# Kernel optimization log

Hardware: AMD Instinct MI355X
Metric: run time of the kernel (lower is better)

Reference implementation:

```python
import jax, jax.numpy as jnp
import numpy as np

B = 4096
D = 512
N_I = 1000000
N_T = 1000000
GAMMA = 0.8
EPS = 1e-10
RHO_I = 8.0
RHO_T = 8.0
ETA_INIT = 1e-05
BETA_U = 0.5
GRAD_CLIP = 5.0
TAU_MIN, TAU_MAX = 0.005, 0.05
TAU_INIT = 0.01


def setup_inputs() -> dict:
    key = jax.random.key(0)
    k1, k2 = jax.random.split(key)
    img = jax.random.normal(k1, (B, D), jnp.float32)
    txt = jax.random.normal(k2, (B, D), jnp.float32)
    # CLIP-style L2-normalized features
    img = img / jnp.linalg.norm(img, axis=1, keepdims=True)
    txt = txt / jnp.linalg.norm(txt, axis=1, keepdims=True)
    return {
        "image_features": img,
        "text_features": txt,
        "s_I": jnp.zeros(N_I, jnp.float32),
        "s_T": jnp.zeros(N_T, jnp.float32),
        "b_I": jnp.zeros(N_I, jnp.float32),
        "b_T": jnp.zeros(N_T, jnp.float32),
        "u_I": jnp.zeros(N_I, jnp.float32),
        "u_T": jnp.zeros(N_T, jnp.float32),
        "tau_I": jnp.full((N_I,), TAU_INIT, jnp.float32),
        "tau_T": jnp.full((N_T,), TAU_INIT, jnp.float32),
        "image_ids": jnp.arange(B, dtype=jnp.int32),
        "text_ids": jnp.arange(B, dtype=jnp.int32),
        "epoch": 1,
    }


def reference(image_features, text_features, s_I, s_T, b_I, b_T, u_I, u_T,
              tau_I, tau_T, image_ids, text_ids, epoch):
    sg = jax.lax.stop_gradient
    sim = jnp.einsum('id,jd->ij', image_features, text_features)  # [B,B]
    diag = jnp.diagonal(sim)
    Bn = sim.shape[0]
    tau_img = tau_I[image_ids]  # [B]
    tau_txt = tau_T[text_ids]   # [B]
    image_diffs = sim - diag[:, None]
    text_diffs = sim - diag[None, :]
    # .detach() in the original -> stop_gradient here
    idt = sg(image_diffs / tau_img[:, None])
    tdt = sg(text_diffs / tau_txt[None, :])
    old_b_I = b_I[image_ids]
    old_b_T = b_T[text_ids]
    # running max for log-sum-exp stabilization
    b_I_row = jnp.maximum(idt.max(axis=1), old_b_I)
    b_T_col = jnp.maximum(tdt.max(axis=0), old_b_T)
    b_I_new = b_I.at[image_ids].set(b_I_row)
    b_T_new = b_T.at[text_ids].set(b_T_col)
    mask = 1.0 - jnp.eye(Bn, dtype=sim.dtype)
    exp_i = jnp.exp(idt - b_I_row[:, None]) * mask
    exp_t = jnp.exp(tdt - b_T_col[None, :]) * mask
    g_I = exp_i.sum(axis=1)
    g_T = exp_t.sum(axis=0)
    if epoch == 0:
        sI = g_I
        sT = g_T
    else:
        sI = (1.0 - GAMMA) * s_I[image_ids] * jnp.exp(old_b_I - b_I_row) + GAMMA * g_I
        sT = (1.0 - GAMMA) * s_T[text_ids] * jnp.exp(old_b_T - b_T_col) + GAMMA * g_T
    s_I_new = s_I.at[image_ids].set(sI)
    s_T_new = s_T.at[text_ids].set(sT)
    w_i = sg(exp_i / (sI[:, None] + EPS))
    w_t = sg(exp_t / (sT[None, :] + EPS))
    image_loss = (w_i * image_diffs).sum(axis=1)
    text_loss = (w_t * text_diffs).sum(axis=0)
    total_loss = image_loss.mean() + text_loss.mean()
    tw_i = jnp.log(sI / (Bn - 1)) + b_I_row + RHO_I - (w_i * idt).sum(axis=1)
    tw_t = jnp.log(sT / (Bn - 1)) + b_T_col + RHO_T - (w_t * tdt).sum(axis=0)
    # torch uses in-place clamp_ on a view, so the returned means are clipped
    tw_i = jnp.clip(tw_i, -GRAD_CLIP, GRAD_CLIP)
    tw_t = jnp.clip(tw_t, -GRAD_CLIP, GRAD_CLIP)
    u_I_val = (1.0 - BETA_U) * u_I[image_ids] + BETA_U * tw_i
    u_T_val = (1.0 - BETA_U) * u_T[text_ids] + BETA_U * tw_t
    u_I_new = u_I.at[image_ids].set(u_I_val)
    u_T_new = u_T.at[text_ids].set(u_T_val)
    tau_I_new = tau_I.at[image_ids].set(jnp.clip(tau_img - ETA_INIT * u_I_val, TAU_MIN, TAU_MAX))
    tau_T_new = tau_T.at[text_ids].set(jnp.clip(tau_txt - ETA_INIT * u_T_val, TAU_MIN, TAU_MAX))
    return (total_loss, tau_img.mean(), tau_txt.mean(), tw_i.mean(), tw_t.mean(),
            s_I_new, s_T_new, b_I_new, b_T_new, u_I_new, u_T_new, tau_I_new, tau_T_new)
```

## Files before the change

kernel.cpp:

```cpp
#include <hip/hip_runtime.h>

typedef unsigned short u16;
typedef unsigned int u32;

typedef __bf16 bf16x8 __attribute__((ext_vector_type(8)));
typedef float floatx4 __attribute__((ext_vector_type(4)));

__device__ __forceinline__ u16 f2bf(float f) {
    union { float f; u32 u; } c; c.f = f;
    u32 u = c.u;
    u32 r = u + 0x7FFFu + ((u >> 16) & 1u);
    return (u16)(r >> 16);
}
__device__ __forceinline__ float bf2f(u16 x) {
    union { u32 u; float f; } c; c.u = ((u32)x) << 16; return c.f;
}

__device__ __forceinline__ void comb(float& M, float& P0, float& P1,
                                     float m, float p0, float p1) {
    float nm = fmaxf(M, m);
    float s = __expf(M - nm), t = __expf(m - nm);
    P0 = P0 * s + p0 * t;
    P1 = P1 * s + p1 * t;
    M = nm;
}

__global__ __launch_bounds__(256) void presplit(
    const float* __restrict__ a, const float* __restrict__ b,
    u16* __restrict__ Ah, u16* __restrict__ Al,
    u16* __restrict__ Bh, u16* __restrict__ Bl, int n,
    const float* __restrict__ tauI, const float* __restrict__ tauT,
    const int* __restrict__ img_ids, const int* __restrict__ txt_ids,
    float* __restrict__ taur, float* __restrict__ tauc) {
    if (blockIdx.y == 0 && blockIdx.x < 16) {
        int t = blockIdx.x * 256 + threadIdx.x;
        taur[t] = tauI[img_ids[t]];
        tauc[t] = tauT[txt_ids[t]];
    }
    const float* src = blockIdx.y ? b : a;
    u16* dh = blockIdx.y ? Bh : Ah;
    u16* dl = blockIdx.y ? Bl : Al;
    int i = (blockIdx.x * 256 + threadIdx.x) * 8;
    if (i >= n) return;
    float4 v0 = *(const float4*)&src[i];
    float4 v1 = *(const float4*)&src[i + 4];
    float xs[8] = {v0.x, v0.y, v0.z, v0.w, v1.x, v1.y, v1.z, v1.w};
    u16 h[8], l[8];
#pragma unroll
    for (int e = 0; e < 8; e++) {
        h[e] = f2bf(xs[e]);
        l[e] = f2bf(xs[e] - bf2f(h[e]));
    }
    int r = i >> 9, k = i & 511;
    int off = (((r >> 4) << 4) + (k >> 5)) * 512 + ((((k >> 3) & 3) << 4) + (r & 15)) * 8;
    *(uint4*)&dh[off] = *(uint4*)h;
    *(uint4*)&dl[off] = *(uint4*)l;
}

#define COPY_BLOCKS 2048

__global__ __launch_bounds__(256) void gemm_flash(
    const u16* __restrict__ Ah, const u16* __restrict__ Al,
    const u16* __restrict__ Bh, const u16* __restrict__ Bl,
    const float* __restrict__ taur, const float* __restrict__ tauc,
    float* __restrict__ rowpart, float* __restrict__ colpart,
    float* __restrict__ diag,
    const float* __restrict__ p0, const float* __restrict__ p1,
    const float* __restrict__ p2, const float* __restrict__ p3,
    const float* __restrict__ p4, const float* __restrict__ p5,
    const float* __restrict__ p6, const float* __restrict__ p7,
    float* __restrict__ out, long long n) {
    __shared__ float redbuf[1536];

    const int bid = blockIdx.x;
    if (bid >= 1024) {
        const int cb = bid - 1024;
        const int k = cb >> 8, blk = cb & 255;
        const float* srcs[8] = {p0, p1, p2, p3, p4, p5, p6, p7};
        const float* src = srcs[k];
        float* dst = out + 5 + (size_t)k * (size_t)n;
        const long long G = (n - 3) >> 2;
        for (long long g = (long long)blk * 256 + threadIdx.x; g < G;
             g += 256 * 256) {
            long long e = 3 + 4 * g;
            float4 q = {src[e], src[e + 1], src[e + 2], src[e + 3]};
            *(float4*)&dst[e] = q;
        }
        if (blk == 0) {
            int t = threadIdx.x;
            long long tail0 = 3 + 4 * G;
            int tcount = (int)(n - tail0);
            if (t < 3) dst[t] = src[t];
            else if (t < 3 + tcount) dst[tail0 + (t - 3)] = src[tail0 + (t - 3)];
        }
        return;
    }

    const int tid  = threadIdx.x;
    const int wave = tid >> 6, lane = tid & 63;
    const int lr = lane & 15, quad = lane >> 4;
    const int waveM = wave >> 1, waveN = wave & 1;
    const int x = bid & 7, s = bid >> 3;
    const int rowtile = (x >> 2) * 16 + (s >> 3);
    const int coltile = (x & 3) * 8 + (s & 7);
    const int rowBase = rowtile * 128;
    const int colBase = coltile * 128;

    const size_t baseA = ((size_t)((rowBase >> 4) + waveM * 4)) * 8192 + lane * 8;
    const size_t baseB = ((size_t)((colBase >> 4) + waveN * 4)) * 8192 + lane * 8;

    floatx4 acc[4][4];
#pragma unroll
    for (int mi = 0; mi < 4; mi++)
#pragma unroll
        for (int ni = 0; ni < 4; ni++) acc[mi][ni] = (floatx4)0.0f;

#pragma unroll 2
    for (int tk = 0; tk < 16; tk++) {
        bf16x8 afh[4], afl[4], bfh[4], bfl[4];
#pragma unroll
        for (int mi = 0; mi < 4; mi++) {
            size_t off = baseA + (size_t)mi * 8192 + tk * 512;
            afh[mi] = *(const bf16x8*)&Ah[off];
            afl[mi] = *(const bf16x8*)&Al[off];
        }
#pragma unroll
        for (int ni = 0; ni < 4; ni++) {
            size_t off = baseB + (size_t)ni * 8192 + tk * 512;
            bfh[ni] = *(const bf16x8*)&Bh[off];
            bfl[ni] = *(const bf16x8*)&Bl[off];
        }
#pragma unroll
        for (int mi = 0; mi < 4; mi++)
#pragma unroll
            for (int ni = 0; ni < 4; ni++) {
                acc[mi][ni] = __builtin_amdgcn_mfma_f32_16x16x32_bf16(afh[mi], bfh[ni], acc[mi][ni], 0, 0, 0);
                acc[mi][ni] = __builtin_amdgcn_mfma_f32_16x16x32_bf16(afh[mi], bfl[ni], acc[mi][ni], 0, 0, 0);
                acc[mi][ni] = __builtin_amdgcn_mfma_f32_16x16x32_bf16(afl[mi], bfh[ni], acc[mi][ni], 0, 0, 0);
            }
    }


    if (rowtile == coltile && waveM == waveN) {
#pragma unroll
        for (int mi = 0; mi < 4; mi++)
#pragma unroll
            for (int r = 0; r < 4; r++)
                if (lr == quad * 4 + r)
                    diag[colBase + waveN * 64 + mi * 16 + lr] = acc[mi][mi][r];
    }

#pragma unroll
    for (int mi = 0; mi < 4; mi++) {
#pragma unroll
        for (int r = 0; r < 4; r++) {
            int row_local = waveM * 64 + mi * 16 + quad * 4 + r;
            float vmax = fmaxf(fmaxf(acc[mi][0][r], acc[mi][1][r]),
                               fmaxf(acc[mi][2][r], acc[mi][3][r]));
#pragma unroll
            for (int mask = 1; mask <= 8; mask <<= 1)
                vmax = fmaxf(vmax, __shfl_xor(vmax, mask));
            float it = 1.0f / taur[rowBase + row_local];
            float M = vmax * it;
            float P0 = 0.f, P1 = 0.f;
#pragma unroll
            for (int ni = 0; ni < 4; ni++) {
                float y = acc[mi][ni][r] * it;
                float e = __expf(y - M);
                P0 += e;
                P1 += y * e;
            }
#pragma unroll
            for (int mask = 1; mask <= 8; mask <<= 1) {
                P0 += __shfl_xor(P0, mask);
                P1 += __shfl_xor(P1, mask);
            }
            if (lr == 0) {
                int xx = (row_local * 2 + waveN) * 3;
                redbuf[xx] = M; redbuf[xx + 1] = P0; redbuf[xx + 2] = P1;
            }
        }
    }

#pragma unroll
    for (int ni = 0; ni < 4; ni++) {
        int col_local = waveN * 64 + ni * 16 + lr;
        float vmax = -3.4e38f;
#pragma unroll
        for (int mi = 0; mi < 4; mi++)
            vmax = fmaxf(vmax,
                fmaxf(fmaxf(acc[mi][ni][0], acc[mi][ni][1]),
                      fmaxf(acc[mi][ni][2], acc[mi][ni][3])));
#pragma unroll
        for (int mask = 16; mask <= 32; mask <<= 1)
            vmax = fmaxf(vmax, __shfl_xor(vmax, mask));
        float it = 1.0f / tauc[colBase + col_local];
        float M = vmax * it;
        float P0 = 0.f, P1 = 0.f;
#pragma unroll
        for (int mi = 0; mi < 4; mi++)
#pragma unroll
            for (int r = 0; r < 4; r++) {
                float y = acc[mi][ni][r] * it;
                float e = __expf(y - M);
                P0 += e;
                P1 += y * e;
            }
#pragma unroll
        for (int mask = 16; mask <= 32; mask <<= 1) {
            P0 += __shfl_xor(P0, mask);
            P1 += __shfl_xor(P1, mask);
        }
        if (quad == 0) {
            int xx = 768 + (col_local * 2 + waveM) * 3;
            redbuf[xx] = M; redbuf[xx + 1] = P0; redbuf[xx + 2] = P1;
        }
    }
    __syncthreads();

    if (tid < 128) {
        int xx = tid * 6;
        float M = redbuf[xx], P0 = redbuf[xx + 1], P1 = redbuf[xx + 2];
        comb(M, P0, P1, redbuf[xx + 3], redbuf[xx + 4], redbuf[xx + 5]);
        float* dst = &rowpart[(size_t)(rowBase + tid) * 96 + coltile * 3];
        dst[0] = M; dst[1] = P0; dst[2] = P1;
    } else {
        int c = tid - 128;
        int xx = 768 + c * 6;
        float M = redbuf[xx], P0 = redbuf[xx + 1], P1 = redbuf[xx + 2];
        comb(M, P0, P1, redbuf[xx + 3], redbuf[xx + 4], redbuf[xx + 5]);
        float* dst = &colpart[(size_t)(colBase + c) * 96 + rowtile * 3];
        dst[0] = M; dst[1] = P0; dst[2] = P1;
    }
}

struct FinArgs {
    const float* rowpart; const float* colpart; const float* diag;
    const float* tauI; const float* sI; const float* bI; const float* uI;
    const float* tauT; const float* sT; const float* bT; const float* uT;
    const int* img_ids; const int* txt_ids; const int* epoch_p;
    float* out; float* rowbuf; long long n;
};

__global__ __launch_bounds__(256) void rows_final(FinArgs a) {
    int t = blockIdx.x * 256 + threadIdx.x;
    int side = t >> 12, i = t & 4095;
    const float* part   = side ? a.colpart : a.rowpart;
    const int*   ids    = side ? a.txt_ids : a.img_ids;
    const float* tau_in = side ? a.tauT : a.tauI;
    const float* s_in   = side ? a.sT   : a.sI;
    const float* b_in   = side ? a.bT   : a.bI;
    const float* u_in   = side ? a.uT   : a.uI;

    const float* p = part + (size_t)i * 96;
    float M = -3.4e38f, P0 = 0.f, P1 = 0.f;
#pragma unroll 4
    for (int k = 0; k < 32; k++)
        comb(M, P0, P1, p[3 * k], p[3 * k + 1], p[3 * k + 2]);

    const int id = ids[i];
    const float tau   = tau_in[id];
    const float old_b = b_in[id];
    const float old_s = s_in[id];
    const float old_u = u_in[id];
    const float y_ii  = a.diag[i] / tau;

    float b_row = fmaxf(M - y_ii, old_b);
    float e  = expf(M - y_ii - b_row);
    float S0 = P0 * e - expf(-b_row);
    float S1 = (P1 - y_ii * P0) * e;

    float g = S0;
    float sI = (*a.epoch_p == 0) ? g
             : 0.2f * old_s * expf(old_b - b_row) + 0.8f * g;
    float denom = sI + 1e-10f;
    float wsum = S1 / denom;
    float lossr = tau * wsum;
    float tw = logf(sI * (1.0f / 4095.0f)) + b_row + 8.0f - wsum;
    tw = fminf(fmaxf(tw, -5.0f), 5.0f);
    float uval = 0.5f * old_u + 0.5f * tw;
    float taun = fminf(fmaxf(tau - 1e-5f * uval, 0.005f), 0.05f);

    float* sect = a.out + 5;
    sect[(size_t)(0 + side) * (size_t)a.n + id] = sI;
    sect[(size_t)(2 + side) * (size_t)a.n + id] = b_row;
    sect[(size_t)(4 + side) * (size_t)a.n + id] = uval;
    sect[(size_t)(6 + side) * (size_t)a.n + id] = taun;

    a.rowbuf[(2 * side + 0) * 4096 + i] = lossr;
    a.rowbuf[(2 * side + 1) * 4096 + i] = tw;
}

__global__ __launch_bounds__(256) void scalars(
    const float* __restrict__ rows,
    const float* __restrict__ tau_I, const float* __restrict__ tau_T,
    const int* __restrict__ image_ids, const int* __restrict__ text_ids,
    float* __restrict__ out) {
    int tid = threadIdx.x;
    int lane = tid & 63, wv = tid >> 6;
    float a[6] = {0, 0, 0, 0, 0, 0};
    for (int e = tid; e < 4096; e += 256) {
        a[0] += rows[0 * 4096 + e];
        a[1] += rows[1 * 4096 + e];
        a[2] += rows[2 * 4096 + e];
        a[3] += rows[3 * 4096 + e];
        a[4] += tau_I[image_ids[e]];
        a[5] += tau_T[text_ids[e]];
    }
    __shared__ float sred[4][6];
#pragma unroll
    for (int k = 0; k < 6; k++)
        for (int o = 32; o > 0; o >>= 1) a[k] += __shfl_xor(a[k], o);
    if (lane == 0)
#pragma unroll
        for (int k = 0; k < 6; k++) sred[wv][k] = a[k];
    __syncthreads();
    if (tid == 0) {
#pragma unroll
        for (int k = 0; k < 6; k++)
            a[k] = sred[0][k] + sred[1][k] + sred[2][k] + sred[3][k];
        const float inv = 1.0f / 4096.0f;
        out[0] = (a[0] + a[2]) * inv;
        out[1] = a[4] * inv;
        out[2] = a[5] * inv;
        out[3] = a[1] * inv;
        out[4] = a[3] * inv;
    }
}

extern "C" void kernel_launch(void* const* d_in, const int* in_sizes, int n_in,
                              void* d_out, int out_size, void* d_ws, size_t ws_size,
                              hipStream_t stream) {
    const float* img   = (const float*)d_in[0];
    const float* txt   = (const float*)d_in[1];
    const float* s_I   = (const float*)d_in[2];
    const float* s_T   = (const float*)d_in[3];
    const float* b_I   = (const float*)d_in[4];
    const float* b_T   = (const float*)d_in[5];
    const float* u_I   = (const float*)d_in[6];
    const float* u_T   = (const float*)d_in[7];
    const float* tau_I = (const float*)d_in[8];
    const float* tau_T = (const float*)d_in[9];
    const int* image_ids = (const int*)d_in[10];
    const int* text_ids  = (const int*)d_in[11];
    const int* epoch     = (const int*)d_in[12];
    float* out = (float*)d_out;
    const long long n = in_sizes[2];
    const int nfeat = in_sizes[0];

    const size_t MB = 1024 * 1024;
    u16* Ah = (u16*)d_ws;
    u16* Al = Ah + (size_t)nfeat;
    u16* Bh = Al + (size_t)nfeat;
    u16* Bl = Bh + (size_t)nfeat;
    float* rowpart = (float*)((char*)d_ws + 16 * MB);
    float* colpart = (float*)((char*)d_ws + 18 * MB);
    float* diag    = (float*)((char*)d_ws + 20 * MB);
    float* taur    = (float*)((char*)d_ws + 20 * MB + 256 * 1024);
    float* tauc    = (float*)((char*)d_ws + 20 * MB + 512 * 1024);
    float* rows    = (float*)((char*)d_ws + 21 * MB);

    presplit<<<dim3((nfeat / 8 + 255) / 256, 2), 256, 0, stream>>>(
        img, txt, Ah, Al, Bh, Bl, nfeat,
        tau_I, tau_T, image_ids, text_ids, taur, tauc);

    gemm_flash<<<1024 + COPY_BLOCKS, 256, 0, stream>>>(
        Ah, Al, Bh, Bl, taur, tauc, rowpart, colpart, diag,
        s_I, s_T, b_I, b_T, u_I, u_T, tau_I, tau_T, out, n);

    FinArgs fa;
    fa.rowpart = rowpart; fa.colpart = colpart; fa.diag = diag;
    fa.tauI = tau_I; fa.sI = s_I; fa.bI = b_I; fa.uI = u_I;
    fa.tauT = tau_T; fa.sT = s_T; fa.bT = b_T; fa.uT = u_T;
    fa.img_ids = image_ids; fa.txt_ids = text_ids; fa.epoch_p = epoch;
    fa.out = out; fa.rowbuf = rows; fa.n = n;
    rows_final<<<32, 256, 0, stream>>>(fa);

    scalars<<<1, 256, 0, stream>>>(rows, tau_I, tau_T, image_ids, text_ids, out);
}
```

Measured before the change: 202.1 us.

## Stage GEMM tiles through LDS and interleave state copy with MFMA loop

Operand tiles for the split-bf16 GEMM are now double-buffered in shared memory using global_load_lds, replacing per-wave direct global loads that each wave fetched redundantly. The separate 2048 copy-only blocks are removed, and the bulk copy of the eight million-entry state arrays is spread across the GEMM blocks' K-loop iterations so its memory traffic overlaps the MFMA work. Launch bounds request two blocks per CU, and the final row reduction loads partials as float4 into registers before combining. The 64KB+ shared footprint and added copy work per block may limit occupancy, and the copy now depends on GEMM progress.

```diff
diff --git a/kernel.cpp b/kernel.cpp
--- a/kernel.cpp
+++ b/kernel.cpp
@@ -23,6 +23,12 @@
     P0 = P0 * s + p0 * t;
     P1 = P1 * s + p1 * t;
     M = nm;
+}
+
+__device__ __forceinline__ void gload16(const void* g, void* l) {
+    __builtin_amdgcn_global_load_lds(
+        (const __attribute__((address_space(1))) void*)g,
+        (__attribute__((address_space(3))) void*)l, 16, 0, 0);
 }
 
 __global__ __launch_bounds__(256) void presplit(
@@ -57,9 +63,7 @@
     *(uint4*)&dl[off] = *(uint4*)l;
 }
 
-#define COPY_BLOCKS 2048
-
-__global__ __launch_bounds__(256) void gemm_flash(
+__global__ __launch_bounds__(256, 2) void gemm_flash(
     const u16* __restrict__ Ah, const u16* __restrict__ Al,
     const u16* __restrict__ Bh, const u16* __restrict__ Bl,
     const float* __restrict__ taur, const float* __restrict__ tauc,
@@ -70,32 +74,10 @@
     const float* __restrict__ p4, const float* __restrict__ p5,
     const float* __restrict__ p6, const float* __restrict__ p7,
     float* __restrict__ out, long long n) {
+    __shared__ u16 tiles[32768];
     __shared__ float redbuf[1536];
 
-    const int bid = blockIdx.x;
-    if (bid >= 1024) {
-        const int cb = bid - 1024;
-        const int k = cb >> 8, blk = cb & 255;
-        const float* srcs[8] = {p0, p1, p2, p3, p4, p5, p6, p7};
-        const float* src = srcs[k];
-        float* dst = out + 5 + (size_t)k * (size_t)n;
-        const long long G = (n - 3) >> 2;
-        for (long long g = (long long)blk * 256 + threadIdx.x; g < G;
-             g += 256 * 256) {
-            long long e = 3 + 4 * g;
-            float4 q = {src[e], src[e + 1], src[e + 2], src[e + 3]};
-            *(float4*)&dst[e] = q;
-        }
-        if (blk == 0) {
-            int t = threadIdx.x;
-            long long tail0 = 3 + 4 * G;
-            int tcount = (int)(n - tail0);
-            if (t < 3) dst[t] = src[t];
-            else if (t < 3 + tcount) dst[tail0 + (t - 3)] = src[tail0 + (t - 3)];
-        }
-        return;
-    }
-
+    const int bid  = blockIdx.x;
     const int tid  = threadIdx.x;
     const int wave = tid >> 6, lane = tid & 63;
     const int lr = lane & 15, quad = lane >> 4;
@@ -106,8 +88,17 @@
     const int rowBase = rowtile * 128;
     const int colBase = coltile * 128;
 
-    const size_t baseA = ((size_t)((rowBase >> 4) + waveM * 4)) * 8192 + lane * 8;
-    const size_t baseB = ((size_t)((colBase >> 4) + waveN * 4)) * 8192 + lane * 8;
+    const u16* gb = (wave == 0) ? Ah : (wave == 1) ? Al : (wave == 2) ? Bh : Bl;
+    const int sbase = (wave < 2) ? rowBase : colBase;
+
+#define STAGE(slice, bufb)                                                    \
+    {                                                                         \
+        _Pragma("unroll")                                                     \
+        for (int j = 0; j < 8; j++) {                                         \
+            size_t ge = ((size_t)(sbase + j * 16 + (slice))) * 512 + lane * 8;\
+            gload16(gb + ge, &tiles[(bufb) + (wave * 8 + j) * 512]);          \
+        }                                                                     \
+    }
 
     floatx4 acc[4][4];
 #pragma unroll
@@ -115,30 +106,75 @@
 #pragma unroll
         for (int ni = 0; ni < 4; ni++) acc[mi][ni] = (floatx4)0.0f;
 
-#pragma unroll 2
-    for (int tk = 0; tk < 16; tk++) {
-        bf16x8 afh[4], afl[4], bfh[4], bfl[4];
-#pragma unroll
-        for (int mi = 0; mi < 4; mi++) {
-            size_t off = baseA + (size_t)mi * 8192 + tk * 512;
-            afh[mi] = *(const bf16x8*)&Ah[off];
-            afl[mi] = *(const bf16x8*)&Al[off];
-        }
-#pragma unroll
-        for (int ni = 0; ni < 4; ni++) {
-            size_t off = baseB + (size_t)ni * 8192 + tk * 512;
-            bfh[ni] = *(const bf16x8*)&Bh[off];
-            bfl[ni] = *(const bf16x8*)&Bl[off];
-        }
-#pragma unroll
-        for (int mi = 0; mi < 4; mi++)
+    const int Gq = (int)((n - 3) >> 2);
+    float* dst5 = out + 5;
+
+    STAGE(0, 0)
+
+    if (bid == 0 && tid < 32) {
+        int arr = tid >> 2, j = tid & 3;
+        const float* sp = (arr & 4) ? ((arr & 2) ? ((arr & 1) ? p7 : p6) : ((arr & 1) ? p5 : p4))
+                                    : ((arr & 2) ? ((arr & 1) ? p3 : p2) : ((arr & 1) ? p1 : p0));
+        float* dp = dst5 + (size_t)arr * (size_t)n;
+        long long tail0 = 3 + 4 * (long long)Gq;
+        if (j < 3) dp[j] = sp[j];
+        else
+            for (long long z = tail0; z < n; z++) dp[z] = sp[z];
+    }
+    __syncthreads();
+
+#pragma unroll 1
+    for (int t = 0; t < 16; t++) {
+        const int cb = (t & 1) << 14;
+        const int nb = cb ^ 16384;
+        if (t < 15) STAGE(t + 1, nb)
+
+        bool docopy = false;
+        float c0 = 0.f, c1 = 0.f, c2 = 0.f, c3 = 0.f;
+        int ck = 0; long long ce = 0;
+        if (t < 8) {
+            int c = bid * 256 + tid + t * 262144;
+            ck = c >> 18;
+            int g = c & 262143;
+            if (g < Gq) {
+                docopy = true;
+                ce = 3 + 4 * (long long)g;
+                const float* sp = (ck & 4) ? ((ck & 2) ? ((ck & 1) ? p7 : p6) : ((ck & 1) ? p5 : p4))
+                                           : ((ck & 2) ? ((ck & 1) ? p3 : p2) : ((ck & 1) ? p1 : p0));
+                c0 = sp[ce]; c1 = sp[ce + 1]; c2 = sp[ce + 2]; c3 = sp[ce + 3];
+            }
+        }
+
+        {
+            const int ab = cb + lane * 8;
+            bf16x8 afh[4], afl[4], bfh[4], bfl[4];
+#pragma unroll
+            for (int mi = 0; mi < 4; mi++) {
+                afh[mi] = *(const bf16x8*)&tiles[ab + (waveM * 4 + mi) * 512];
+                afl[mi] = *(const bf16x8*)&tiles[ab + (8 + waveM * 4 + mi) * 512];
+            }
 #pragma unroll
             for (int ni = 0; ni < 4; ni++) {
-                acc[mi][ni] = __builtin_amdgcn_mfma_f32_16x16x32_bf16(afh[mi], bfh[ni], acc[mi][ni], 0, 0, 0);
-                acc[mi][ni] = __builtin_amdgcn_mfma_f32_16x16x32_bf16(afh[mi], bfl[ni], acc[mi][ni], 0, 0, 0);
-                acc[mi][ni] = __builtin_amdgcn_mfma_f32_16x16x32_bf16(afl[mi], bfh[ni], acc[mi][ni], 0, 0, 0);
-            }
-    }
+                bfh[ni] = *(const bf16x8*)&tiles[ab + (16 + waveN * 4 + ni) * 512];
+                bfl[ni] = *(const bf16x8*)&tiles[ab + (24 + waveN * 4 + ni) * 512];
+            }
+#pragma unroll
+            for (int mi = 0; mi < 4; mi++)
+#pragma unroll
+                for (int ni = 0; ni < 4; ni++) {
+                    acc[mi][ni] = __builtin_amdgcn_mfma_f32_16x16x32_bf16(afh[mi], bfh[ni], acc[mi][ni], 0, 0, 0);
+                    acc[mi][ni] = __builtin_amdgcn_mfma_f32_16x16x32_bf16(afh[mi], bfl[ni], acc[mi][ni], 0, 0, 0);
+                    acc[mi][ni] = __builtin_amdgcn_mfma_f32_16x16x32_bf16(afl[mi], bfh[ni], acc[mi][ni], 0, 0, 0);
+                }
+        }
+
+        if (docopy) {
+            float4 q = {c0, c1, c2, c3};
+            *(float4*)&dst5[(size_t)ck * (size_t)n + ce] = q;
+        }
+        __syncthreads();
+    }
+#undef STAGE
 
 
     if (rowtile == coltile && waveM == waveN) {
@@ -252,18 +288,29 @@
     const float* b_in   = side ? a.bT   : a.bI;
     const float* u_in   = side ? a.uT   : a.uI;
 
-    const float* p = part + (size_t)i * 96;
+    const int id = ids[i];
+    const float dg = a.diag[i];
+
+    const float4* p4 = (const float4*)(part + (size_t)i * 96);
+    float v[96];
+#pragma unroll
+    for (int k = 0; k < 24; k++) {
+        float4 q = p4[k];
+        v[4 * k]     = q.x;
+        v[4 * k + 1] = q.y;
+        v[4 * k + 2] = q.z;
+        v[4 * k + 3] = q.w;
+    }
     float M = -3.4e38f, P0 = 0.f, P1 = 0.f;
-#pragma unroll 4
+#pragma unroll
     for (int k = 0; k < 32; k++)
-        comb(M, P0, P1, p[3 * k], p[3 * k + 1], p[3 * k + 2]);
-
-    const int id = ids[i];
+        comb(M, P0, P1, v[3 * k], v[3 * k + 1], v[3 * k + 2]);
+
     const float tau   = tau_in[id];
     const float old_b = b_in[id];
     const float old_s = s_in[id];
     const float old_u = u_in[id];
-    const float y_ii  = a.diag[i] / tau;
+    const float y_ii  = dg / tau;
 
     float b_row = fmaxf(M - y_ii, old_b);
     float e  = expf(M - y_ii - b_row);
@@ -364,7 +411,7 @@
         img, txt, Ah, Al, Bh, Bl, nfeat,
         tau_I, tau_T, image_ids, text_ids, taur, tauc);
 
-    gemm_flash<<<1024 + COPY_BLOCKS, 256, 0, stream>>>(
+    gemm_flash<<<1024, 256, 0, stream>>>(
         Ah, Al, Bh, Bl, taur, tauc, rowpart, colpart, diag,
         s_I, s_T, b_I, b_T, u_I, u_T, tau_I, tau_T, out, n);
 
```

Result: faster. 192.9 us (-4.6%).
